# Kernel tuning notes

Hardware: AMD Instinct MI355X
Metric: run time of the kernel (lower is better)

The kernel has to match this reference:

```python
import jax, jax.numpy as jnp
import numpy as np

N_NODES = 50000
N_EDGES = 800000
N_GRAPHS = 512
K_HOPS = 2


def setup_inputs() -> dict:
    key = jax.random.key(0)
    ks = jax.random.split(key, 6)
    x = jax.random.normal(ks[0], (N_NODES, 75), dtype=jnp.float32)
    edge_index = jax.random.randint(ks[1], (2, N_EDGES), 0, N_NODES, dtype=jnp.int64)
    batch = jnp.sort(jax.random.randint(ks[2], (N_NODES,), 0, N_GRAPHS, dtype=jnp.int64))
    # Glorot-ish init for linear layers
    W1 = jax.random.normal(ks[3], (75, 128), dtype=jnp.float32) * (1.0 / np.sqrt(75))
    b1 = jnp.zeros((128,), dtype=jnp.float32)
    W2 = jax.random.normal(ks[4], (128, 1), dtype=jnp.float32) * (1.0 / np.sqrt(128))
    b2 = jnp.zeros((1,), dtype=jnp.float32)
    return {"x": x, "edge_index": edge_index, "batch": batch,
            "W1": W1, "b1": b1, "W2": W2, "b2": b2}


def _sgc_forward(x, edge_index, batch, W1, b1, W2, b2):
    N = x.shape[0]
    # gcn_norm with added self-loops (PyG SGConv default)
    loop = jnp.arange(N, dtype=edge_index.dtype)
    row = jnp.concatenate([edge_index[0], loop])
    col = jnp.concatenate([edge_index[1], loop])
    w = jnp.ones(row.shape[0], dtype=x.dtype)
    deg = jax.ops.segment_sum(w, col, num_segments=N)
    deg_inv_sqrt = jnp.where(deg > 0, jax.lax.rsqrt(jnp.maximum(deg, 1e-12)), 0.0)
    norm = deg_inv_sqrt[row] * deg_inv_sqrt[col]  # [E+N]
    # K hops of normalized sparse propagation: out[col] += norm * x[row]
    for _ in range(K_HOPS):
        x = jax.ops.segment_sum(norm[:, None] * x[row], col, num_segments=N)
    # SGConv final linear
    h = x @ W1 + b1  # [N,128]
    # global_add_pool: segment sum by graph id
    pooled = jax.ops.segment_sum(h, batch, num_segments=N_GRAPHS)  # [G,128]
    return pooled @ W2 + b2  # [G,1]


def reference(x, edge_index, batch, W1, b1, W2, b2):
    return _sgc_forward(x, edge_index, batch, W1, b1, W2, b2)
```

## Files before the change

### kernel.cpp

```cpp
#include <hip/hip_runtime.h>


#define N_    50000
#define E_    800000
#define G_    512
#define F_    75
#define H_    128
#define RR    256
#define BWR   196
#define PBLK  256
#define EPB   3125
#define SLOT  40
#define SEGW  16

struct Pr {
    const float* x; const int* row; const int* col; const int* batch;
    const float* W1; const float* b1; const float* W2; const float* b2;
    float* u; float2* kd; float* cbw; int* bcnt; int* bcnt2;
    unsigned* ebuf; unsigned* ebuf2; float* out;
};

__global__ __launch_bounds__(1024)
void k1_part(Pr p) {
    const int t = threadIdx.x, b = blockIdx.x;
    __shared__ __align__(16) unsigned st1[RR * SLOT];
    __shared__ __align__(16) unsigned st2[RR * SLOT];
    __shared__ int wc[RR], wc2[RR];
    if (t < RR) { wc[t] = 0; wc2[t] = 0; }
    if (b == 0) {
        if (t >= 512 && t < 1024) p.out[t - 512] = p.b2[0];
        if (t == 500) {
            float s = 0.f;
            #pragma unroll 8
            for (int j = 0; j < H_; ++j) s += p.b1[j] * p.W2[j];
            p.cbw[0] = s;
        }
    }
    __syncthreads();
    const int e0 = b * EPB;
    for (int e = e0 + t; e < e0 + EPB; e += 1024) {
        int cv = p.col[e];
        int rv = p.row[e];
        int r = cv / BWR;
        int k = atomicAdd(&wc[r], 1);
        if (k < SLOT)
            st1[r * SLOT + k] = ((unsigned)rv << 8) | (unsigned)(cv - r * BWR);
        int r2 = rv / BWR;
        int k2 = atomicAdd(&wc2[r2], 1);
        if (k2 < SLOT)
            st2[r2 * SLOT + k2] = ((unsigned)cv << 8) | (unsigned)(rv - r2 * BWR);
    }
    __syncthreads();
    {
        const int rg = t >> 2, sub = t & 3;
        int c1 = wc[rg];  if (c1 > SLOT) c1 = SLOT;
        int c2 = wc2[rg]; if (c2 > SLOT) c2 = SLOT;
        uint4* d1 = (uint4*)(p.ebuf  + (size_t)b * RR * SLOT + rg * SLOT);
        uint4* d2 = (uint4*)(p.ebuf2 + (size_t)b * RR * SLOT + rg * SLOT);
        const uint4* s1 = (const uint4*)(st1 + rg * SLOT);
        const uint4* s2 = (const uint4*)(st2 + rg * SLOT);
        for (int i = sub; i * 4 < c1; i += 4) d1[i] = s1[i];
        for (int i = sub; i * 4 < c2; i += 4) d2[i] = s2[i];
        if (sub == 0) {
            p.bcnt[rg * PBLK + b]  = c1;
            p.bcnt2[rg * PBLK + b] = c2;
        }
    }
}

__global__ __launch_bounds__(1024)
void k2_deg(Pr p) {
    const int t = threadIdx.x, r = blockIdx.x;
    __shared__ float xs[BWR * F_];
    __shared__ float sv[F_ + 1];
    __shared__ float bins[BWR];
    __shared__ int scnt[PBLK];
    if (t < F_) {
        float s = 0.f;
        #pragma unroll 8
        for (int j = 0; j < H_; ++j) s += p.W1[t * H_ + j] * p.W2[j];
        sv[t] = s;
    }
    if (t < BWR) bins[t] = 0.f;
    if (t < PBLK) scnt[t] = p.bcnt[r * PBLK + t];
    __syncthreads();
    const int n0 = r * BWR;
    int rem = N_ - n0; if (rem > BWR) rem = BWR; if (rem < 0) rem = 0;
    const int nf4 = rem * F_ / 4;
    const float4* xsrc = (const float4*)(p.x + (size_t)n0 * F_);
    for (int i = t; i < nf4; i += 1024) ((float4*)xs)[i] = xsrc[i];
    const int w = t >> 6, lane = t & 63;
    #pragma unroll
    for (int i = 0; i < SEGW; ++i) {
        int b = w * SEGW + i;
        if (lane < scnt[b]) {
            unsigned wd = p.ebuf[(size_t)(b * RR + r) * SLOT + lane];
            atomicAdd(&bins[wd & 255u], 1.0f);
        }
    }
    __syncthreads();
    const int ln = t >> 2, part = t & 3;
    if (ln < rem) {
        const float* xr = xs + ln * F_;
        float s = 0.f;
        for (int j = part; j < F_; j += 4) s += xr[j] * sv[j];
        s += __shfl_xor(s, 1);
        s += __shfl_xor(s, 2);
        if (part == 0) {
            int node = n0 + ln;
            float d = rsqrtf(bins[ln] + 1.0f);
            p.kd[node] = make_float2(d, __int_as_float(p.batch[node]));
            p.u[node] = d * s;
        }
    }
}

__global__ __launch_bounds__(1024)
void k3_hop(Pr p) {
    const int t = threadIdx.x, r = blockIdx.x;
    __shared__ float bins[BWR];
    __shared__ float h[G_];
    __shared__ int scnt[PBLK], scnt2[PBLK];
    if (t < BWR) bins[t] = 0.f;
    for (int i = t; i < G_; i += 1024) h[i] = 0.f;
    if (t < PBLK) {
        scnt[t]  = p.bcnt[r * PBLK + t];
        scnt2[t] = p.bcnt2[r * PBLK + t];
    }
    __syncthreads();
    const int w = t >> 6, lane = t & 63;
    #pragma unroll
    for (int i = 0; i < SEGW; ++i) {
        int b = w * SEGW + i;
        if (lane < scnt[b]) {
            unsigned wd = p.ebuf[(size_t)(b * RR + r) * SLOT + lane];
            atomicAdd(&bins[wd & 255u], p.u[wd >> 8]);
        }
    }
    __syncthreads();
    if (t < 256) {
        float val = 0.f; int g = -1;
        int node = r * BWR + t;
        if (t < BWR && node < N_) {
            float2 k = p.kd[node];
            float nu = k.x * k.x * (bins[t] + p.u[node]);
            bins[t] = nu;
            val = k.x * nu + p.cbw[0];
            g = __float_as_int(k.y);
        }
        int g0 = __shfl(g, 0), g63 = __shfl(g, 63);
        if (g0 == g63 && g0 >= 0) {
            for (int o = 32; o; o >>= 1) val += __shfl_down(val, o);
            if ((t & 63) == 0) atomicAdd(&h[g0], val);
        } else if (g >= 0) {
            atomicAdd(&h[g], val);
        }
    }
    __syncthreads();
    #pragma unroll
    for (int i = 0; i < SEGW; ++i) {
        int b = w * SEGW + i;
        if (lane < scnt2[b]) {
            unsigned wd = p.ebuf2[(size_t)(b * RR + r) * SLOT + lane];
            float2 k = p.kd[wd >> 8];
            atomicAdd(&h[__float_as_int(k.y)], k.x * bins[wd & 255u]);
        }
    }
    __syncthreads();
    for (int i = t; i < G_; i += 1024)
        if (h[i] != 0.f) atomicAdd(&p.out[i], h[i]);
}

__global__ void f_setup(const float* W1, const float* b1, const float* W2,
                        const float* b2, float* v, float* cb) {
    int t = threadIdx.x;
    if (t < F_) {
        float s = 0.f;
        for (int j = 0; j < H_; ++j) s += W1[t * H_ + j] * W2[j];
        v[t] = s;
    } else if (t == F_) {
        float s = 0.f;
        for (int j = 0; j < H_; ++j) s += b1[j] * W2[j];
        cb[0] = s; cb[1] = b2[0];
    }
}
__global__ void f_init(float* deg, float* s, int n) {
    int i = blockIdx.x * blockDim.x + threadIdx.x;
    if (i < n) { deg[i] = 1.0f; s[i] = 0.0f; }
}
__global__ void f_deg_acc(const int* __restrict__ col, float* deg, int e) {
    int i = blockIdx.x * blockDim.x + threadIdx.x;
    if (i < e) atomicAdd(&deg[col[i]], 1.0f);
}
__global__ void f_dis(float* deg, int n) {
    int i = blockIdx.x * blockDim.x + threadIdx.x;
    if (i < n) deg[i] = rsqrtf(deg[i]);
}
__global__ void f_u0(const float* __restrict__ x, const float* __restrict__ v,
                     const float* __restrict__ dis, float* u, int n) {
    __shared__ float sv[F_];
    if (threadIdx.x < F_) sv[threadIdx.x] = v[threadIdx.x];
    __syncthreads();
    int i = blockIdx.x * blockDim.x + threadIdx.x;
    if (i < n) {
        const float* xi = x + (size_t)i * F_;
        float s = 0.f;
        for (int j = 0; j < F_; ++j) s += xi[j] * sv[j];
        u[i] = dis[i] * s;
    }
}
__global__ void f_edge(const int* __restrict__ row, const int* __restrict__ col,
                       const float* __restrict__ u, float* s, int e) {
    int i = blockIdx.x * blockDim.x + threadIdx.x;
    if (i < e) atomicAdd(&s[col[i]], u[row[i]]);
}
__global__ void f_hop_finish(const float* __restrict__ dis, float* s, float* u, int n) {
    int i = blockIdx.x * blockDim.x + threadIdx.x;
    if (i < n) { float d = dis[i]; u[i] = d * d * (s[i] + u[i]); s[i] = 0.0f; }
}
__global__ void f_out_init(const float* __restrict__ cb, float* out, int g) {
    int i = blockIdx.x * blockDim.x + threadIdx.x;
    if (i < g) out[i] = cb[1];
}
__global__ void f_pool(const int* __restrict__ batch, const float* __restrict__ dis,
                       const float* __restrict__ s, const float* __restrict__ u,
                       const float* __restrict__ cb, float* out, int n) {
    int i = blockIdx.x * blockDim.x + threadIdx.x;
    if (i < n) atomicAdd(&out[batch[i]], dis[i] * (s[i] + u[i]) + cb[0]);
}

extern "C" void kernel_launch(void* const* d_in, const int* in_sizes, int n_in,
                              void* d_out, int out_size, void* d_ws, size_t ws_size,
                              hipStream_t stream) {
    const float* x   = (const float*)d_in[0];
    const int*   ei  = (const int*)d_in[1];
    const int*   bat = (const int*)d_in[2];
    const float* W1  = (const float*)d_in[3];
    const float* b1  = (const float*)d_in[4];
    const float* W2  = (const float*)d_in[5];
    const float* b2  = (const float*)d_in[6];
    float* out = (float*)d_out;

    float* ws = (float*)d_ws;
    Pr p;
    p.x = x; p.row = ei; p.col = ei + E_; p.batch = bat;
    p.W1 = W1; p.b1 = b1; p.W2 = W2; p.b2 = b2;
    p.u     = ws;
    p.kd    = (float2*)(ws + N_);
    p.cbw   = ws + 3 * N_;
    p.bcnt  = (int*)(p.cbw + 8);
    p.bcnt2 = p.bcnt + RR * PBLK;
    p.ebuf  = (unsigned*)(p.bcnt2 + RR * PBLK);
    p.ebuf2 = p.ebuf + (size_t)PBLK * RR * SLOT;
    p.out   = out;

    const size_t need = ((size_t)3 * N_ + 8 + 2 * (size_t)RR * PBLK * (1 + SLOT))
                        * sizeof(float);

    if (ws_size >= need) {
        k1_part<<<PBLK, 1024, 0, stream>>>(p);
        k2_deg<<<RR, 1024, 0, stream>>>(p);
        k3_hop<<<RR, 1024, 0, stream>>>(p);
    } else {
        float* v  = ws;
        float* cb = ws + 128;
        float* dis = ws + 136;
        float* u  = dis + N_;
        float* s  = u + N_;
        const int B = 256;
        const int gN = (N_ + B - 1) / B;
        const int gE = (E_ + B - 1) / B;
        f_setup<<<1, 128, 0, stream>>>(W1, b1, W2, b2, v, cb);
        f_init<<<gN, B, 0, stream>>>(dis, s, N_);
        f_deg_acc<<<gE, B, 0, stream>>>(ei + E_, dis, E_);
        f_dis<<<gN, B, 0, stream>>>(dis, N_);
        f_u0<<<gN, B, 0, stream>>>(x, v, dis, u, N_);
        f_edge<<<gE, B, 0, stream>>>(ei, ei + E_, u, s, E_);
        f_hop_finish<<<gN, B, 0, stream>>>(dis, s, u, N_);
        f_out_init<<<1, G_, 0, stream>>>(cb, out, G_);
        f_edge<<<gE, B, 0, stream>>>(ei, ei + E_, u, s, E_);
        f_pool<<<gN, B, 0, stream>>>(bat, dis, s, u, cb, out, N_);
    }
}
```

Before: 51.07 us.

## Compact partitioned edge buckets into contiguous per-bucket buffers via global cursors

Edge partitioning now reserves space in one contiguous buffer per destination bucket, using a global atomicAdd cursor per bucket, instead of fixed per-(block, bucket) slots with separate counts. Each reservation is padded to a multiple of 4 with dummy entries. The degree and hop kernels can then stream each bucket's edges with all threads in a flat strided loop. This removes the sparse 64-lane slot scans, where most lanes sat idle, and the per-block count loads. In exchange it adds a memset launch, global atomics per block and bucket in the partition kernel, and a fixed per-bucket capacity that silently drops edges if it overflows.

Measured after the change: 55.94 us. 9.5% more time.

```diff
diff --git a/kernel.cpp b/kernel.cpp
--- a/kernel.cpp
+++ b/kernel.cpp
@@ -11,12 +11,12 @@
 #define PBLK  256
 #define EPB   3125
 #define SLOT  40
-#define SEGW  16
+#define CAPR  4096
 
 struct Pr {
     const float* x; const int* row; const int* col; const int* batch;
     const float* W1; const float* b1; const float* W2; const float* b2;
-    float* u; float2* kd; float* cbw; int* bcnt; int* bcnt2;
+    float* u; float2* kd; float* cbw; int* cur1; int* cur2;
     unsigned* ebuf; unsigned* ebuf2; float* out;
 };
 
@@ -25,7 +25,7 @@
     const int t = threadIdx.x, b = blockIdx.x;
     __shared__ __align__(16) unsigned st1[RR * SLOT];
     __shared__ __align__(16) unsigned st2[RR * SLOT];
-    __shared__ int wc[RR], wc2[RR];
+    __shared__ int wc[RR], wc2[RR], base1[RR], base2[RR];
     if (t < RR) { wc[t] = 0; wc2[t] = 0; }
     if (b == 0) {
         if (t >= 512 && t < 1024) p.out[t - 512] = p.b2[0];
@@ -51,19 +51,33 @@
             st2[r2 * SLOT + k2] = ((unsigned)cv << 8) | (unsigned)(rv - r2 * BWR);
     }
     __syncthreads();
+    if (t < RR) {
+        int c1 = wc[t];  if (c1 > SLOT) c1 = SLOT;
+        int c1r = (c1 + 3) & ~3;
+        for (int i = c1; i < c1r; ++i) st1[t * SLOT + i] = 255u;
+        int bb = atomicAdd(&p.cur1[t], c1r);
+        base1[t] = (bb + c1r <= CAPR) ? bb : -1;
+        wc[t] = c1r;
+        int c2 = wc2[t]; if (c2 > SLOT) c2 = SLOT;
+        int c2r = (c2 + 3) & ~3;
+        for (int i = c2; i < c2r; ++i) st2[t * SLOT + i] = 255u;
+        bb = atomicAdd(&p.cur2[t], c2r);
+        base2[t] = (bb + c2r <= CAPR) ? bb : -1;
+        wc2[t] = c2r;
+    }
+    __syncthreads();
     {
         const int rg = t >> 2, sub = t & 3;
-        int c1 = wc[rg];  if (c1 > SLOT) c1 = SLOT;
-        int c2 = wc2[rg]; if (c2 > SLOT) c2 = SLOT;
-        uint4* d1 = (uint4*)(p.ebuf  + (size_t)b * RR * SLOT + rg * SLOT);
-        uint4* d2 = (uint4*)(p.ebuf2 + (size_t)b * RR * SLOT + rg * SLOT);
+        int c1r = wc[rg], c2r = wc2[rg];
         const uint4* s1 = (const uint4*)(st1 + rg * SLOT);
         const uint4* s2 = (const uint4*)(st2 + rg * SLOT);
-        for (int i = sub; i * 4 < c1; i += 4) d1[i] = s1[i];
-        for (int i = sub; i * 4 < c2; i += 4) d2[i] = s2[i];
-        if (sub == 0) {
-            p.bcnt[rg * PBLK + b]  = c1;
-            p.bcnt2[rg * PBLK + b] = c2;
+        if (base1[rg] >= 0) {
+            uint4* d1 = (uint4*)(p.ebuf + (size_t)rg * CAPR + base1[rg]);
+            for (int i = sub; i * 4 < c1r; i += 4) d1[i] = s1[i];
+        }
+        if (base2[rg] >= 0) {
+            uint4* d2 = (uint4*)(p.ebuf2 + (size_t)rg * CAPR + base2[rg]);
+            for (int i = sub; i * 4 < c2r; i += 4) d2[i] = s2[i];
         }
     }
 }
@@ -73,31 +87,24 @@
     const int t = threadIdx.x, r = blockIdx.x;
     __shared__ float xs[BWR * F_];
     __shared__ float sv[F_ + 1];
-    __shared__ float bins[BWR];
-    __shared__ int scnt[PBLK];
+    __shared__ float bins[256];
     if (t < F_) {
         float s = 0.f;
         #pragma unroll 8
         for (int j = 0; j < H_; ++j) s += p.W1[t * H_ + j] * p.W2[j];
         sv[t] = s;
     }
-    if (t < BWR) bins[t] = 0.f;
-    if (t < PBLK) scnt[t] = p.bcnt[r * PBLK + t];
+    if (t < 256) bins[t] = 0.f;
     __syncthreads();
     const int n0 = r * BWR;
     int rem = N_ - n0; if (rem > BWR) rem = BWR; if (rem < 0) rem = 0;
     const int nf4 = rem * F_ / 4;
     const float4* xsrc = (const float4*)(p.x + (size_t)n0 * F_);
     for (int i = t; i < nf4; i += 1024) ((float4*)xs)[i] = xsrc[i];
-    const int w = t >> 6, lane = t & 63;
-    #pragma unroll
-    for (int i = 0; i < SEGW; ++i) {
-        int b = w * SEGW + i;
-        if (lane < scnt[b]) {
-            unsigned wd = p.ebuf[(size_t)(b * RR + r) * SLOT + lane];
-            atomicAdd(&bins[wd & 255u], 1.0f);
-        }
-    }
+    int cnt = p.cur1[r]; if (cnt > CAPR) cnt = CAPR;
+    const unsigned* eb = p.ebuf + (size_t)r * CAPR;
+    for (int j = t; j < cnt; j += 1024)
+        atomicAdd(&bins[eb[j] & 255u], 1.0f);
     __syncthreads();
     const int ln = t >> 2, part = t & 3;
     if (ln < rem) {
@@ -118,22 +125,16 @@
 __global__ __launch_bounds__(1024)
 void k3_hop(Pr p) {
     const int t = threadIdx.x, r = blockIdx.x;
-    __shared__ float bins[BWR];
+    __shared__ float bins[256];
     __shared__ float h[G_];
-    __shared__ int scnt[PBLK], scnt2[PBLK];
-    if (t < BWR) bins[t] = 0.f;
+    if (t < 256) bins[t] = 0.f;
     for (int i = t; i < G_; i += 1024) h[i] = 0.f;
-    if (t < PBLK) {
-        scnt[t]  = p.bcnt[r * PBLK + t];
-        scnt2[t] = p.bcnt2[r * PBLK + t];
-    }
-    __syncthreads();
-    const int w = t >> 6, lane = t & 63;
-    #pragma unroll
-    for (int i = 0; i < SEGW; ++i) {
-        int b = w * SEGW + i;
-        if (lane < scnt[b]) {
-            unsigned wd = p.ebuf[(size_t)(b * RR + r) * SLOT + lane];
+    __syncthreads();
+    {
+        int cnt = p.cur1[r]; if (cnt > CAPR) cnt = CAPR;
+        const unsigned* eb = p.ebuf + (size_t)r * CAPR;
+        for (int j = t; j < cnt; j += 1024) {
+            unsigned wd = eb[j];
             atomicAdd(&bins[wd & 255u], p.u[wd >> 8]);
         }
     }
@@ -147,6 +148,8 @@
             bins[t] = nu;
             val = k.x * nu + p.cbw[0];
             g = __float_as_int(k.y);
+        } else {
+            bins[t] = 0.f;
         }
         int g0 = __shfl(g, 0), g63 = __shfl(g, 63);
         if (g0 == g63 && g0 >= 0) {
@@ -157,11 +160,11 @@
         }
     }
     __syncthreads();
-    #pragma unroll
-    for (int i = 0; i < SEGW; ++i) {
-        int b = w * SEGW + i;
-        if (lane < scnt2[b]) {
-            unsigned wd = p.ebuf2[(size_t)(b * RR + r) * SLOT + lane];
+    {
+        int cnt = p.cur2[r]; if (cnt > CAPR) cnt = CAPR;
+        const unsigned* eb2 = p.ebuf2 + (size_t)r * CAPR;
+        for (int j = t; j < cnt; j += 1024) {
+            unsigned wd = eb2[j];
             float2 k = p.kd[wd >> 8];
             atomicAdd(&h[__float_as_int(k.y)], k.x * bins[wd & 255u]);
         }
@@ -248,16 +251,17 @@
     p.u     = ws;
     p.kd    = (float2*)(ws + N_);
     p.cbw   = ws + 3 * N_;
-    p.bcnt  = (int*)(p.cbw + 8);
-    p.bcnt2 = p.bcnt + RR * PBLK;
-    p.ebuf  = (unsigned*)(p.bcnt2 + RR * PBLK);
-    p.ebuf2 = p.ebuf + (size_t)PBLK * RR * SLOT;
+    p.cur1  = (int*)(p.cbw + 8);
+    p.cur2  = p.cur1 + RR;
+    p.ebuf  = (unsigned*)(p.cur2 + RR);
+    p.ebuf2 = p.ebuf + (size_t)RR * CAPR;
     p.out   = out;
 
-    const size_t need = ((size_t)3 * N_ + 8 + 2 * (size_t)RR * PBLK * (1 + SLOT))
+    const size_t need = ((size_t)3 * N_ + 8 + 2 * RR + 2 * (size_t)RR * CAPR)
                         * sizeof(float);
 
     if (ws_size >= need) {
+        hipMemsetAsync(p.cur1, 0, 2 * RR * sizeof(int), stream);
         k1_part<<<PBLK, 1024, 0, stream>>>(p);
         k2_deg<<<RR, 1024, 0, stream>>>(p);
         k3_hop<<<RR, 1024, 0, stream>>>(p);
```
